# Performance work log

Hardware: AMD Instinct MI355X
Metric: run time of the kernel (lower is better)

Reference implementation:

```python
import jax, jax.numpy as jnp
import numpy as np

EMB = 64

def _segment_mean(x, ids, num_segments):
    s = jax.ops.segment_sum(x, ids, num_segments=num_segments)
    c = jax.ops.segment_sum(jnp.ones((ids.shape[0], 1), x.dtype), ids, num_segments=num_segments)
    return s / jnp.maximum(c, 1.0)

def setup_inputs() -> dict:
    key = jax.random.key(0)
    ks = jax.random.split(key, 8)
    E, N, G = 800000, 50000, 16
    edge_distance_vec = jax.random.normal(ks[0], (E, 3), dtype=jnp.float32)
    x_edge = jax.random.normal(ks[1], (E, EMB), dtype=jnp.float32)
    edge_index = jax.random.randint(ks[2], (E,), 0, N, dtype=jnp.int64)
    batch = jnp.sort(jax.random.randint(ks[3], (N,), 0, G, dtype=jnp.int64))
    # MLP params (torch Linear: y = x @ W.T + b); store as [in, out]
    lim1 = 1.0 / np.sqrt(EMB)
    W1 = jax.random.uniform(ks[4], (EMB, EMB), jnp.float32, -lim1, lim1)
    b1 = jax.random.uniform(ks[5], (EMB,), jnp.float32, -lim1, lim1)
    W2 = jax.random.uniform(ks[6], (EMB, 1), jnp.float32, -lim1, lim1)
    b2 = jax.random.uniform(ks[7], (1,), jnp.float32, -lim1, lim1)
    return {"edge_distance_vec": edge_distance_vec, "x_edge": x_edge,
            "edge_index": edge_index, "batch": batch,
            "n_nodes": N, "n_graphs": G,
            "W1": W1, "b1": b1, "W2": W2, "b2": b2}

def reference(edge_distance_vec, x_edge, edge_index, batch, n_nodes, n_graphs, W1, b1, W2, b2):
    E = edge_distance_vec.shape[0]
    # outer product of edge vectors -> [E, 9]
    outer = (edge_distance_vec[:, :, None] * edge_distance_vec[:, None, :]).reshape(E, 9)
    # edge_outer = x_edge[:, :, None] * outer[:, None, :] -> transpose(1,2) -> [E, 9, emb]
    edge_outer = outer[:, :, None] * x_edge[:, None, :]
    # per-edge, per-component MLP: Linear(emb,emb) -> SiLU -> Linear(emb,1)
    h = jax.nn.silu(jnp.einsum('eci,io->eco', edge_outer, W1) + b1)
    edge_out = (jnp.einsum('eci,io->eco', h, W2) + b2).reshape(E, 9)
    # scatter-mean edge -> node, then node -> graph (non-extensive)
    node_outer = _segment_mean(edge_out, edge_index, n_nodes)
    stress = _segment_mean(node_outer, batch, n_graphs)
    return stress
```

## Files before the change

kernel.cpp:

```cpp
#include <hip/hip_runtime.h>

#define EMB  64
#define NREP 256

typedef __attribute__((ext_vector_type(8))) short bf16x8;
typedef __attribute__((ext_vector_type(4))) float f32x4;
union BF8 { bf16x8 v; short s[8]; };

static __device__ __forceinline__ short f2bf(float f) {
    unsigned u = __float_as_uint(f);
    u += 0x7fffu + ((u >> 16) & 1u);
    return (short)(u >> 16);
}

__global__ __launch_bounds__(256) void prep_kernel(
    const int* __restrict__ eidx, int* __restrict__ ecnt, int E,
    const int* __restrict__ batch, int* __restrict__ gStart, int N)
{
    int t = blockIdx.x * 256 + threadIdx.x;
    if (t < N) {
        int g = batch[t];
        if (t == 0 || batch[t - 1] != g) gStart[g] = t;
    }
    if (t < E) atomicAdd(&ecnt[eidx[t]], 1);
}

__global__ __launch_bounds__(256, 4) void edge_kernel(
    const float* __restrict__ dvec, const float* __restrict__ x_edge,
    const int*   __restrict__ eidx, const int* __restrict__ batch,
    const int*   __restrict__ ecnt,
    const float* __restrict__ W1, const float* __restrict__ b1,
    const float* __restrict__ W2, const float* __restrict__ b2,
    float* __restrict__ repsum, int E)
{
    __shared__ float bins[96];
    __shared__ float sb1[64], sw2[64];
    const int tid = threadIdx.x;
    if (tid < 96) bins[tid] = 0.f;
    if (tid < 64) { sb1[tid] = b1[tid]; sw2[tid] = W2[tid]; }
    __syncthreads();

    const int lane = tid & 63, wave = tid >> 6;
    const int col  = lane & 15, quad = lane >> 4;

    BF8 Af[4][2];
    #pragma unroll
    for (int mt = 0; mt < 4; ++mt)
        #pragma unroll
        for (int kt = 0; kt < 2; ++kt) {
            const float* wp = W1 + (kt * 32 + quad * 8) * 64 + mt * 16 + col;
            #pragma unroll
            for (int j = 0; j < 8; ++j) Af[mt][kt].s[j] = f2bf(wp[j * 64]);
        }

    const float NL2E = -1.442695040888963f;
    const float bb2  = b2[0];
    const long  ebase = (long)blockIdx.x * 256 + wave * 64;

    #pragma unroll 1
    for (int nt = 0; nt < 4; ++nt) {
        long e = ebase + nt * 16 + col;
        bool valid = (e < E);
        if (!valid) e = 0;

        int   n = 0; float scale = 0.f; int g = 0;
        if (quad < 2) {
            n = eidx[e];
            scale = 1.0f / (float)max(ecnt[n], 1);
            g = batch[n];
        }

        const float* xp = x_edge + (size_t)e * EMB + quad * 8;
        f32x4 xa = *(const f32x4*)(xp);
        f32x4 xb = *(const f32x4*)(xp + 4);
        f32x4 xc = *(const f32x4*)(xp + 32);
        f32x4 xd = *(const f32x4*)(xp + 36);
        BF8 B0, B1;
        B0.s[0] = f2bf(xa.x); B0.s[1] = f2bf(xa.y); B0.s[2] = f2bf(xa.z); B0.s[3] = f2bf(xa.w);
        B0.s[4] = f2bf(xb.x); B0.s[5] = f2bf(xb.y); B0.s[6] = f2bf(xb.z); B0.s[7] = f2bf(xb.w);
        B1.s[0] = f2bf(xc.x); B1.s[1] = f2bf(xc.y); B1.s[2] = f2bf(xc.z); B1.s[3] = f2bf(xc.w);
        B1.s[4] = f2bf(xd.x); B1.s[5] = f2bf(xd.y); B1.s[6] = f2bf(xd.z); B1.s[7] = f2bf(xd.w);

        float d0 = dvec[3 * e + 0];
        float d1 = dvec[3 * e + 1];
        float d2 = dvec[3 * e + 2];
        float a[6] = { d0 * d0, d1 * d1, d2 * d2, d0 * d1, d0 * d2, d1 * d2 };

        float acc[6] = { 0.f, 0.f, 0.f, 0.f, 0.f, 0.f };

        #pragma unroll
        for (int mt = 0; mt < 4; ++mt) {
            f32x4 D = { 0.f, 0.f, 0.f, 0.f };
            D = __builtin_amdgcn_mfma_f32_16x16x32_bf16(Af[mt][0].v, B0.v, D, 0, 0, 0);
            D = __builtin_amdgcn_mfma_f32_16x16x32_bf16(Af[mt][1].v, B1.v, D, 0, 0, 0);
            #pragma unroll
            for (int r = 0; r < 4; ++r) {
                int   o  = mt * 16 + quad * 4 + r;
                float y  = D[r];
                float b  = sb1[o];
                float w2 = sw2[o];
                #pragma unroll
                for (int c = 0; c < 6; ++c) {
                    float z  = fmaf(a[c], y, b);
                    float ex = __builtin_amdgcn_exp2f(z * NL2E);
                    float rr = __builtin_amdgcn_rcpf(1.0f + ex);
                    acc[c]   = fmaf(w2, z * rr, acc[c]);
                }
            }
        }

        #pragma unroll
        for (int c = 0; c < 6; ++c) {
            acc[c] += __shfl_xor(acc[c], 16, 64);
            acc[c] += __shfl_xor(acc[c], 32, 64);
        }

        if (valid && quad < 2) {
            #pragma unroll
            for (int j = 0; j < 3; ++j) {
                int c = quad * 3 + j;
                atomicAdd(&bins[g * 6 + c], (acc[c] + bb2) * scale);
            }
        }
    }

    __syncthreads();
    if (tid < 96) {
        int rep = blockIdx.x & (NREP - 1);
        atomicAdd(repsum + (size_t)rep * 96 + tid, bins[tid]);
    }
}

__global__ __launch_bounds__(384) void final_kernel(
    const float* __restrict__ repsum, const int* __restrict__ gStart,
    float* __restrict__ out, int N)
{
    __shared__ float part[4][96];
    __shared__ float sh[96];
    __shared__ int gs[17];
    int t = threadIdx.x;
    int r0 = t / 96, gc = t % 96;
    float s = 0.f;
    #pragma unroll 8
    for (int r = r0; r < NREP; r += 4) s += repsum[(size_t)r * 96 + gc];
    part[r0][gc] = s;
    if (t == 0) {
        gs[16] = N;
        for (int g = 15; g >= 0; --g) {
            unsigned v = (unsigned)gStart[g];
            gs[g] = (v > (unsigned)gs[g + 1]) ? gs[g + 1] : (int)v;
        }
    }
    __syncthreads();
    if (t < 96) sh[t] = part[0][t] + part[1][t] + part[2][t] + part[3][t];
    __syncthreads();
    if (t < 16) {
        int gN = gs[t + 1] - gs[t];
        float inv = 1.0f / fmaxf((float)gN, 1.0f);
        float m0 = sh[t * 6 + 0] * inv;
        float m1 = sh[t * 6 + 1] * inv;
        float m2 = sh[t * 6 + 2] * inv;
        float m3 = sh[t * 6 + 3] * inv;
        float m4 = sh[t * 6 + 4] * inv;
        float m5 = sh[t * 6 + 5] * inv;
        float* p = out + t * 9;
        p[0] = m0; p[1] = m3; p[2] = m4;
        p[3] = m3; p[4] = m1; p[5] = m5;
        p[6] = m4; p[7] = m5; p[8] = m2;
    }
}

extern "C" void kernel_launch(void* const* d_in, const int* in_sizes, int n_in,
                              void* d_out, int out_size, void* d_ws, size_t ws_size,
                              hipStream_t stream) {
    const float* dvec   = (const float*)d_in[0];
    const float* x_edge = (const float*)d_in[1];
    const int*   eidx   = (const int*)d_in[2];
    const int*   batch  = (const int*)d_in[3];
    const float* W1     = (const float*)d_in[6];
    const float* b1     = (const float*)d_in[7];
    const float* W2     = (const float*)d_in[8];
    const float* b2     = (const float*)d_in[9];

    int E = in_sizes[0] / 3;
    int N = in_sizes[3];

    int*   ecnt   = (int*)d_ws;
    float* repsum = (float*)(ecnt + N);
    int*   gStart = (int*)(repsum + (size_t)NREP * 96);

    hipMemsetAsync(d_ws, 0, ((size_t)N + (size_t)NREP * 96) * 4, stream);
    hipMemsetAsync(gStart, 0xFF, 17 * 4, stream);

    int blocks = (E + 255) / 256;
    prep_kernel<<<blocks, 256, 0, stream>>>(eidx, ecnt, E, batch, gStart, N);
    edge_kernel<<<blocks, 256, 0, stream>>>(dvec, x_edge, eidx, batch, ecnt,
                                            W1, b1, W2, b2, repsum, E);
    final_kernel<<<1, 384, 0, stream>>>(repsum, gStart, (float*)d_out, N);
}
```

Measured before the change: 399.9 us.

## Fuse prep, edge and final kernels into one persistent kernel with grid barriers

Merges the three kernel launches into a single persistent kernel sized to the device's resident-block capacity. Edge counting and graph-start detection run first, followed by a software grid barrier, then the edge MLP loops over tiles. A second barrier precedes block 0 computing the final reduction. This removes two launch gaps and the separate final kernel, at the cost of spin-wait barriers, host occupancy queries on every call, and reliance on all blocks being co-resident.

```diff
diff --git a/kernel.cpp b/kernel.cpp
--- a/kernel.cpp
+++ b/kernel.cpp
@@ -13,32 +13,35 @@
     return (short)(u >> 16);
 }
 
-__global__ __launch_bounds__(256) void prep_kernel(
-    const int* __restrict__ eidx, int* __restrict__ ecnt, int E,
-    const int* __restrict__ batch, int* __restrict__ gStart, int N)
-{
-    int t = blockIdx.x * 256 + threadIdx.x;
-    if (t < N) {
-        int g = batch[t];
-        if (t == 0 || batch[t - 1] != g) gStart[g] = t;
-    }
-    if (t < E) atomicAdd(&ecnt[eidx[t]], 1);
-}
-
-__global__ __launch_bounds__(256, 4) void edge_kernel(
+static __device__ __forceinline__ void grid_barrier(int* cnt, int nb) {
+    __syncthreads();
+    if (threadIdx.x == 0) {
+        __threadfence();
+        __hip_atomic_fetch_add(cnt, 1, __ATOMIC_RELEASE, __HIP_MEMORY_SCOPE_AGENT);
+        while (__hip_atomic_load(cnt, __ATOMIC_RELAXED, __HIP_MEMORY_SCOPE_AGENT) < nb)
+            __builtin_amdgcn_s_sleep(2);
+        __threadfence();
+    }
+    __syncthreads();
+}
+
+__global__ __launch_bounds__(256, 4) void fused_kernel(
     const float* __restrict__ dvec, const float* __restrict__ x_edge,
     const int*   __restrict__ eidx, const int* __restrict__ batch,
-    const int*   __restrict__ ecnt,
     const float* __restrict__ W1, const float* __restrict__ b1,
     const float* __restrict__ W2, const float* __restrict__ b2,
-    float* __restrict__ repsum, int E)
+    int* __restrict__ ecnt, float* __restrict__ repsum,
+    int* __restrict__ gStart, int* __restrict__ barcnt,
+    float* __restrict__ out, int E, int N, int nb, int tiles)
 {
     __shared__ float bins[96];
     __shared__ float sb1[64], sw2[64];
+    __shared__ float sh[96];
+    __shared__ int   gs[17];
+
     const int tid = threadIdx.x;
     if (tid < 96) bins[tid] = 0.f;
     if (tid < 64) { sb1[tid] = b1[tid]; sw2[tid] = W2[tid]; }
-    __syncthreads();
 
     const int lane = tid & 63, wave = tid >> 6;
     const int col  = lane & 15, quad = lane >> 4;
@@ -53,73 +56,82 @@
             for (int j = 0; j < 8; ++j) Af[mt][kt].s[j] = f2bf(wp[j * 64]);
         }
 
+    const int gt = blockIdx.x * 256 + tid, gsz = nb * 256;
+    for (int t = gt; t < E; t += gsz) atomicAdd(&ecnt[eidx[t]], 1);
+    for (int t = gt; t < N; t += gsz) {
+        int g = batch[t];
+        if (t == 0 || batch[t - 1] != g) gStart[g] = t;
+    }
+    grid_barrier(&barcnt[0], nb);
+
     const float NL2E = -1.442695040888963f;
     const float bb2  = b2[0];
-    const long  ebase = (long)blockIdx.x * 256 + wave * 64;
-
-    #pragma unroll 1
-    for (int nt = 0; nt < 4; ++nt) {
-        long e = ebase + nt * 16 + col;
-        bool valid = (e < E);
-        if (!valid) e = 0;
-
-        int   n = 0; float scale = 0.f; int g = 0;
-        if (quad < 2) {
-            n = eidx[e];
-            scale = 1.0f / (float)max(ecnt[n], 1);
-            g = batch[n];
-        }
-
-        const float* xp = x_edge + (size_t)e * EMB + quad * 8;
-        f32x4 xa = *(const f32x4*)(xp);
-        f32x4 xb = *(const f32x4*)(xp + 4);
-        f32x4 xc = *(const f32x4*)(xp + 32);
-        f32x4 xd = *(const f32x4*)(xp + 36);
-        BF8 B0, B1;
-        B0.s[0] = f2bf(xa.x); B0.s[1] = f2bf(xa.y); B0.s[2] = f2bf(xa.z); B0.s[3] = f2bf(xa.w);
-        B0.s[4] = f2bf(xb.x); B0.s[5] = f2bf(xb.y); B0.s[6] = f2bf(xb.z); B0.s[7] = f2bf(xb.w);
-        B1.s[0] = f2bf(xc.x); B1.s[1] = f2bf(xc.y); B1.s[2] = f2bf(xc.z); B1.s[3] = f2bf(xc.w);
-        B1.s[4] = f2bf(xd.x); B1.s[5] = f2bf(xd.y); B1.s[6] = f2bf(xd.z); B1.s[7] = f2bf(xd.w);
-
-        float d0 = dvec[3 * e + 0];
-        float d1 = dvec[3 * e + 1];
-        float d2 = dvec[3 * e + 2];
-        float a[6] = { d0 * d0, d1 * d1, d2 * d2, d0 * d1, d0 * d2, d1 * d2 };
-
-        float acc[6] = { 0.f, 0.f, 0.f, 0.f, 0.f, 0.f };
-
-        #pragma unroll
-        for (int mt = 0; mt < 4; ++mt) {
-            f32x4 D = { 0.f, 0.f, 0.f, 0.f };
-            D = __builtin_amdgcn_mfma_f32_16x16x32_bf16(Af[mt][0].v, B0.v, D, 0, 0, 0);
-            D = __builtin_amdgcn_mfma_f32_16x16x32_bf16(Af[mt][1].v, B1.v, D, 0, 0, 0);
+
+    for (int tile = blockIdx.x; tile < tiles; tile += nb) {
+        const long ebase = (long)tile * 256 + wave * 64;
+        #pragma unroll 1
+        for (int nt = 0; nt < 4; ++nt) {
+            long e = ebase + nt * 16 + col;
+            bool valid = (e < E);
+            if (!valid) e = 0;
+
+            int g = 0; float scale = 0.f;
+            if (quad < 2) {
+                int n = eidx[e];
+                scale = 1.0f / (float)max(ecnt[n], 1);
+                g = batch[n];
+            }
+
+            const float* xp = x_edge + (size_t)e * EMB + quad * 8;
+            f32x4 xa = *(const f32x4*)(xp);
+            f32x4 xb = *(const f32x4*)(xp + 4);
+            f32x4 xc = *(const f32x4*)(xp + 32);
+            f32x4 xd = *(const f32x4*)(xp + 36);
+            BF8 B0, B1;
+            B0.s[0] = f2bf(xa.x); B0.s[1] = f2bf(xa.y); B0.s[2] = f2bf(xa.z); B0.s[3] = f2bf(xa.w);
+            B0.s[4] = f2bf(xb.x); B0.s[5] = f2bf(xb.y); B0.s[6] = f2bf(xb.z); B0.s[7] = f2bf(xb.w);
+            B1.s[0] = f2bf(xc.x); B1.s[1] = f2bf(xc.y); B1.s[2] = f2bf(xc.z); B1.s[3] = f2bf(xc.w);
+            B1.s[4] = f2bf(xd.x); B1.s[5] = f2bf(xd.y); B1.s[6] = f2bf(xd.z); B1.s[7] = f2bf(xd.w);
+
+            float d0 = dvec[3 * e + 0];
+            float d1 = dvec[3 * e + 1];
+            float d2 = dvec[3 * e + 2];
+            float a[6] = { d0 * d0, d1 * d1, d2 * d2, d0 * d1, d0 * d2, d1 * d2 };
+            float acc[6] = { 0.f, 0.f, 0.f, 0.f, 0.f, 0.f };
+
             #pragma unroll
-            for (int r = 0; r < 4; ++r) {
-                int   o  = mt * 16 + quad * 4 + r;
-                float y  = D[r];
-                float b  = sb1[o];
-                float w2 = sw2[o];
+            for (int mt = 0; mt < 4; ++mt) {
+                f32x4 D = { 0.f, 0.f, 0.f, 0.f };
+                D = __builtin_amdgcn_mfma_f32_16x16x32_bf16(Af[mt][0].v, B0.v, D, 0, 0, 0);
+                D = __builtin_amdgcn_mfma_f32_16x16x32_bf16(Af[mt][1].v, B1.v, D, 0, 0, 0);
                 #pragma unroll
-                for (int c = 0; c < 6; ++c) {
-                    float z  = fmaf(a[c], y, b);
-                    float ex = __builtin_amdgcn_exp2f(z * NL2E);
-                    float rr = __builtin_amdgcn_rcpf(1.0f + ex);
-                    acc[c]   = fmaf(w2, z * rr, acc[c]);
+                for (int r = 0; r < 4; ++r) {
+                    int   o  = mt * 16 + quad * 4 + r;
+                    float y  = D[r];
+                    float b  = sb1[o];
+                    float w2 = sw2[o];
+                    #pragma unroll
+                    for (int c = 0; c < 6; ++c) {
+                        float z  = fmaf(a[c], y, b);
+                        float ex = __builtin_amdgcn_exp2f(z * NL2E);
+                        float rr = __builtin_amdgcn_rcpf(1.0f + ex);
+                        acc[c]   = fmaf(w2, z * rr, acc[c]);
+                    }
                 }
             }
-        }
-
-        #pragma unroll
-        for (int c = 0; c < 6; ++c) {
-            acc[c] += __shfl_xor(acc[c], 16, 64);
-            acc[c] += __shfl_xor(acc[c], 32, 64);
-        }
-
-        if (valid && quad < 2) {
+
             #pragma unroll
-            for (int j = 0; j < 3; ++j) {
-                int c = quad * 3 + j;
-                atomicAdd(&bins[g * 6 + c], (acc[c] + bb2) * scale);
+            for (int c = 0; c < 6; ++c) {
+                acc[c] += __shfl_xor(acc[c], 16, 64);
+                acc[c] += __shfl_xor(acc[c], 32, 64);
+            }
+
+            if (valid && quad < 2) {
+                #pragma unroll
+                for (int j = 0; j < 3; ++j) {
+                    int c = quad * 3 + j;
+                    atomicAdd(&bins[g * 6 + c], (acc[c] + bb2) * scale);
+                }
             }
         }
     }
@@ -129,44 +141,37 @@
         int rep = blockIdx.x & (NREP - 1);
         atomicAdd(repsum + (size_t)rep * 96 + tid, bins[tid]);
     }
-}
-
-__global__ __launch_bounds__(384) void final_kernel(
-    const float* __restrict__ repsum, const int* __restrict__ gStart,
-    float* __restrict__ out, int N)
-{
-    __shared__ float part[4][96];
-    __shared__ float sh[96];
-    __shared__ int gs[17];
-    int t = threadIdx.x;
-    int r0 = t / 96, gc = t % 96;
-    float s = 0.f;
-    #pragma unroll 8
-    for (int r = r0; r < NREP; r += 4) s += repsum[(size_t)r * 96 + gc];
-    part[r0][gc] = s;
-    if (t == 0) {
-        gs[16] = N;
-        for (int g = 15; g >= 0; --g) {
-            unsigned v = (unsigned)gStart[g];
-            gs[g] = (v > (unsigned)gs[g + 1]) ? gs[g + 1] : (int)v;
-        }
-    }
-    __syncthreads();
-    if (t < 96) sh[t] = part[0][t] + part[1][t] + part[2][t] + part[3][t];
-    __syncthreads();
-    if (t < 16) {
-        int gN = gs[t + 1] - gs[t];
-        float inv = 1.0f / fmaxf((float)gN, 1.0f);
-        float m0 = sh[t * 6 + 0] * inv;
-        float m1 = sh[t * 6 + 1] * inv;
-        float m2 = sh[t * 6 + 2] * inv;
-        float m3 = sh[t * 6 + 3] * inv;
-        float m4 = sh[t * 6 + 4] * inv;
-        float m5 = sh[t * 6 + 5] * inv;
-        float* p = out + t * 9;
-        p[0] = m0; p[1] = m3; p[2] = m4;
-        p[3] = m3; p[4] = m1; p[5] = m5;
-        p[6] = m4; p[7] = m5; p[8] = m2;
+    grid_barrier(&barcnt[16], nb);
+
+    if (blockIdx.x == 0) {
+        if (tid < 96) {
+            float s = 0.f;
+            #pragma unroll 8
+            for (int r = 0; r < NREP; ++r) s += repsum[(size_t)r * 96 + tid];
+            sh[tid] = s;
+        }
+        if (tid == 0) {
+            gs[16] = N;
+            for (int g = 15; g >= 0; --g) {
+                unsigned v = (unsigned)gStart[g];
+                gs[g] = (v > (unsigned)gs[g + 1]) ? gs[g + 1] : (int)v;
+            }
+        }
+        __syncthreads();
+        if (tid < 16) {
+            int gN = gs[tid + 1] - gs[tid];
+            float inv = 1.0f / fmaxf((float)gN, 1.0f);
+            float m0 = sh[tid * 6 + 0] * inv;
+            float m1 = sh[tid * 6 + 1] * inv;
+            float m2 = sh[tid * 6 + 2] * inv;
+            float m3 = sh[tid * 6 + 3] * inv;
+            float m4 = sh[tid * 6 + 4] * inv;
+            float m5 = sh[tid * 6 + 5] * inv;
+            float* p = out + tid * 9;
+            p[0] = m0; p[1] = m3; p[2] = m4;
+            p[3] = m3; p[4] = m1; p[5] = m5;
+            p[6] = m4; p[7] = m5; p[8] = m2;
+        }
     }
 }
 
@@ -187,14 +192,28 @@
 
     int*   ecnt   = (int*)d_ws;
     float* repsum = (float*)(ecnt + N);
-    int*   gStart = (int*)(repsum + (size_t)NREP * 96);
-
-    hipMemsetAsync(d_ws, 0, ((size_t)N + (size_t)NREP * 96) * 4, stream);
-    hipMemsetAsync(gStart, 0xFF, 17 * 4, stream);
-
-    int blocks = (E + 255) / 256;
-    prep_kernel<<<blocks, 256, 0, stream>>>(eidx, ecnt, E, batch, gStart, N);
-    edge_kernel<<<blocks, 256, 0, stream>>>(dvec, x_edge, eidx, batch, ecnt,
-                                            W1, b1, W2, b2, repsum, E);
-    final_kernel<<<1, 384, 0, stream>>>(repsum, gStart, (float*)d_out, N);
-}
+    int*   barcnt = (int*)(repsum + (size_t)NREP * 96);
+    int*   gStart = barcnt + 32;
+
+    size_t zero_elems = (size_t)N + (size_t)NREP * 96 + 32;
+    hipMemsetAsync(d_ws, 0, zero_elems * 4, stream);
+    hipMemsetAsync(gStart, 0xFF, 16 * 4, stream);
+
+    int occ = 0;
+    hipOccupancyMaxActiveBlocksPerMultiprocessor(
+        &occ, reinterpret_cast<const void*>(fused_kernel), 256, 0);
+    if (occ < 1) occ = 1;
+    int ncu = 0;
+    hipDeviceGetAttribute(&ncu, hipDeviceAttributeMultiprocessorCount, 0);
+    if (ncu <= 0) ncu = 256;
+
+    int tiles = (E + 255) / 256;
+    long maxb = (long)occ * ncu;
+    int tpb = (int)((tiles + maxb - 1) / maxb);
+    int nb  = (tiles + tpb - 1) / tpb;
+
+    fused_kernel<<<nb, 256, 0, stream>>>(dvec, x_edge, eidx, batch,
+                                         W1, b1, W2, b2,
+                                         ecnt, repsum, gStart, barcnt,
+                                         (float*)d_out, E, N, nb, tiles);
+}
```

After: 524.7 us. 1.31x slower.
